# Kernel tuning notes

Measured on AMD Instinct MI355X. Metric: run time of the kernel, lower is better.

Reference implementation:

```python
import jax, jax.numpy as jnp
import numpy as np

D_MODEL = 1024
NHEAD = 16
HEAD_DIM = D_MODEL // NHEAD


def setup_inputs() -> dict:
    key = jax.random.key(0)
    kx, kw1, kb1, kw2, kb2 = jax.random.split(key, 5)
    x = jax.random.normal(kx, (4, 2048, D_MODEL), dtype=jnp.float32)
    s = 1.0 / np.sqrt(D_MODEL)
    W_qkv = jax.random.uniform(kw1, (D_MODEL, 3 * D_MODEL), jnp.float32, -s, s)
    b_qkv = jax.random.uniform(kb1, (3 * D_MODEL,), jnp.float32, -s, s)
    W_out = jax.random.uniform(kw2, (D_MODEL, D_MODEL), jnp.float32, -s, s)
    b_out = jax.random.uniform(kb2, (D_MODEL,), jnp.float32, -s, s)
    return {"x": x, "W_qkv": W_qkv, "b_qkv": b_qkv, "W_out": W_out, "b_out": b_out}


def reference(x, W_qkv, b_qkv, W_out, b_out):
    B, S, _ = x.shape
    scale = HEAD_DIM ** -0.5
    qkv = x @ W_qkv + b_qkv                               # [B,S,3*D]
    qkv = qkv.reshape(B, S, 3, NHEAD, HEAD_DIM)
    qkv = jnp.transpose(qkv, (2, 0, 3, 1, 4))             # [3,B,H,S,Dh]
    q, k, v = qkv[0], qkv[1], qkv[2]
    scores = jnp.einsum('bhsd,bhtd->bhst', q, k) * scale  # [B,H,S,S]
    attn = jax.nn.softmax(scores, axis=-1)
    out = jnp.einsum('bhst,bhtd->bhsd', attn, v)          # [B,H,S,Dh]
    out = jnp.transpose(out, (0, 2, 1, 3)).reshape(B, S, D_MODEL)
    return out @ W_out + b_out
```

## Files before the change

kernel.cpp:

```cpp
#include <hip/hip_runtime.h>
#include <hip/hip_bf16.h>

#define SEQ 2048
#define BATCH 4
#define DMODEL 1024
#define NHEAD 16

#define QK_SCALE_LOG2E 0.1803368801111137f

typedef __attribute__((ext_vector_type(8))) __bf16 bf16x8;
typedef __attribute__((ext_vector_type(4))) __bf16 bf16x4;
typedef __attribute__((ext_vector_type(4))) float f32x4;

__device__ __forceinline__ void gload_lds16(const void* g, void* l) {
    __builtin_amdgcn_global_load_lds(
        (const __attribute__((address_space(1))) void*)g,
        (__attribute__((address_space(3))) void*)l, 16, 0, 0);
}

__global__ __launch_bounds__(256) void cast_f32_to_bf16(
    const float* __restrict__ in, __bf16* __restrict__ out, int n4)
{
    int i = blockIdx.x * 256 + threadIdx.x;
    if (i >= n4) return;
    float4 v = reinterpret_cast<const float4*>(in)[i];
    bf16x4 o = { (__bf16)v.x, (__bf16)v.y, (__bf16)v.z, (__bf16)v.w };
    reinterpret_cast<bf16x4*>(out)[i] = o;
}

__global__ __launch_bounds__(256) void trans_w(
    const float* __restrict__ W, __bf16* __restrict__ WT, int K, int N)
{
    __shared__ float t[32][33];
    const int tid = threadIdx.x;
    const int n0 = blockIdx.x * 32, k0 = blockIdx.y * 32;
    const int tx = tid & 31, ty = tid >> 5;
    #pragma unroll
    for (int j = 0; j < 4; ++j)
        t[ty + 8*j][tx] = W[(size_t)(k0 + ty + 8*j) * N + n0 + tx];
    __syncthreads();
    #pragma unroll
    for (int j = 0; j < 4; ++j)
        WT[(size_t)(n0 + ty + 8*j) * K + k0 + tx] = (__bf16)t[tx][ty + 8*j];
}

__global__ __launch_bounds__(256) void gemm_qkv(
    const __bf16* __restrict__ A, const __bf16* __restrict__ BT,
    const float* __restrict__ bias,
    __bf16* __restrict__ Qb, __bf16* __restrict__ Kt, __bf16* __restrict__ Vt,
    int M, int N, int K)
{
    __shared__ __attribute__((aligned(128))) char As[2][8192];
    __shared__ __attribute__((aligned(128))) char Bs[2][8192];

    const int tid = threadIdx.x, wv = tid >> 6, ln = tid & 63;
    const int nwg = gridDim.x * gridDim.y;
    const int bid = blockIdx.y * gridDim.x + blockIdx.x;
    const int swz = (bid & 7) * (nwg >> 3) + (bid >> 3);
    const int rowBase = (swz / gridDim.x) * 128;
    const int colBase = (swz % gridDim.x) * 128;

    const int mq = (wv >> 1) * 64, nq = (wv & 1) * 64;
    const int lg = ln >> 4, lc = ln & 15;
    const int srow = ln >> 2;
    const int skoff = (ln & 3) * 8;

    const __bf16* asrc0 = A  + (size_t)(rowBase + (wv*2+0)*16 + srow) * K + skoff;
    const __bf16* asrc1 = A  + (size_t)(rowBase + (wv*2+1)*16 + srow) * K + skoff;
    const __bf16* bsrc0 = BT + (size_t)(colBase + (wv*2+0)*16 + srow) * K + skoff;
    const __bf16* bsrc1 = BT + (size_t)(colBase + (wv*2+1)*16 + srow) * K + skoff;

    #define GSTAGE(kt, buf) do {                                      \
        gload_lds16(asrc0 + (kt) * 32, As[buf] + (wv*2+0)*1024);      \
        gload_lds16(asrc1 + (kt) * 32, As[buf] + (wv*2+1)*1024);      \
        gload_lds16(bsrc0 + (kt) * 32, Bs[buf] + (wv*2+0)*1024);      \
        gload_lds16(bsrc1 + (kt) * 32, Bs[buf] + (wv*2+1)*1024);      \
    } while (0)

    const int nkt = K / 32;
    GSTAGE(0, 0);
    GSTAGE(1, 1);

    f32x4 acc[4][4] = {};

    for (int kt = 0; kt < nkt; ++kt) {
        const int cur = kt & 1;
        asm volatile("s_waitcnt vmcnt(4)" ::: "memory");
        __builtin_amdgcn_s_barrier();

        bf16x8 af[4], bf[4];
        #pragma unroll
        for (int m = 0; m < 4; ++m)
            af[m] = *(const bf16x8*)(As[cur] + (mq + m*16 + lc) * 64 + lg * 16);
        #pragma unroll
        for (int n = 0; n < 4; ++n)
            bf[n] = *(const bf16x8*)(Bs[cur] + (nq + n*16 + lc) * 64 + lg * 16);
        #pragma unroll
        for (int m = 0; m < 4; ++m)
            #pragma unroll
            for (int n = 0; n < 4; ++n)
                acc[m][n] = __builtin_amdgcn_mfma_f32_16x16x32_bf16(af[m], bf[n], acc[m][n], 0, 0, 0);

        __builtin_amdgcn_s_barrier();
        int cn = kt + 2;
        if (cn > nkt - 1) cn = nkt - 1;
        GSTAGE(cn, cur);
    }
    asm volatile("s_waitcnt vmcnt(0)" ::: "memory");
    #undef GSTAGE

    #pragma unroll
    for (int m = 0; m < 4; ++m) {
        int row0 = rowBase + mq + m * 16 + lg * 4;
        int b = row0 >> 11, s0 = row0 & 2047;
        #pragma unroll
        for (int n = 0; n < 4; ++n) {
            int col = colBase + nq + n * 16 + lc;
            float bv = bias[col];
            if (colBase < DMODEL) {
                #pragma unroll
                for (int r = 0; r < 4; ++r)
                    Qb[(size_t)(row0 + r) * DMODEL + col] =
                        (__bf16)((acc[m][n][r] + bv) * QK_SCALE_LOG2E);
            } else if (colBase < 2 * DMODEL) {
                int h = (col >> 6) & 15, d = col & 63;
                __bf16* kp = &Kt[((size_t)(b * 16 + h) * SEQ + s0) * 64 + d];
                #pragma unroll
                for (int r = 0; r < 4; ++r)
                    kp[r * 64] = (__bf16)(acc[m][n][r] + bv);
            } else {
                int h = (col >> 6) & 15, d = col & 63;
                int sp = (s0 & ~63) | (s0 & 32) | ((s0 & 12) << 1) | ((s0 & 16) >> 2);
                bf16x4 vv = { (__bf16)(acc[m][n][0] + bv), (__bf16)(acc[m][n][1] + bv),
                              (__bf16)(acc[m][n][2] + bv), (__bf16)(acc[m][n][3] + bv) };
                *(bf16x4*)&Vt[((size_t)(b * 16 + h) * 64 + d) * SEQ + sp] = vv;
            }
        }
    }
}

__global__ __launch_bounds__(256) void gemm_out(
    const __bf16* __restrict__ A, const __bf16* __restrict__ BT,
    const float* __restrict__ bias, float* __restrict__ Cout,
    int M, int N, int K)
{
    __shared__ __attribute__((aligned(128))) char As[2][8192];
    __shared__ __attribute__((aligned(128))) char Bs[2][8192];

    const int tid = threadIdx.x, wv = tid >> 6, ln = tid & 63;
    const int nwg = gridDim.x * gridDim.y;
    const int bid = blockIdx.y * gridDim.x + blockIdx.x;
    const int swz = (bid & 7) * (nwg >> 3) + (bid >> 3);
    const int rowBase = (swz / gridDim.x) * 128;
    const int colBase = (swz % gridDim.x) * 128;

    const int mq = (wv >> 1) * 64, nq = (wv & 1) * 64;
    const int lg = ln >> 4, lc = ln & 15;
    const int srow = ln >> 2;
    const int skoff = (ln & 3) * 8;

    const __bf16* asrc0 = A  + (size_t)(rowBase + (wv*2+0)*16 + srow) * K + skoff;
    const __bf16* asrc1 = A  + (size_t)(rowBase + (wv*2+1)*16 + srow) * K + skoff;
    const __bf16* bsrc0 = BT + (size_t)(colBase + (wv*2+0)*16 + srow) * K + skoff;
    const __bf16* bsrc1 = BT + (size_t)(colBase + (wv*2+1)*16 + srow) * K + skoff;

    #define GSTAGE(kt, buf) do {                                      \
        gload_lds16(asrc0 + (kt) * 32, As[buf] + (wv*2+0)*1024);      \
        gload_lds16(asrc1 + (kt) * 32, As[buf] + (wv*2+1)*1024);      \
        gload_lds16(bsrc0 + (kt) * 32, Bs[buf] + (wv*2+0)*1024);      \
        gload_lds16(bsrc1 + (kt) * 32, Bs[buf] + (wv*2+1)*1024);      \
    } while (0)

    const int nkt = K / 32;
    GSTAGE(0, 0);
    GSTAGE(1, 1);

    f32x4 acc[4][4] = {};

    for (int kt = 0; kt < nkt; ++kt) {
        const int cur = kt & 1;
        asm volatile("s_waitcnt vmcnt(4)" ::: "memory");
        __builtin_amdgcn_s_barrier();

        bf16x8 af[4], bf[4];
        #pragma unroll
        for (int m = 0; m < 4; ++m)
            af[m] = *(const bf16x8*)(As[cur] + (mq + m*16 + lc) * 64 + lg * 16);
        #pragma unroll
        for (int n = 0; n < 4; ++n)
            bf[n] = *(const bf16x8*)(Bs[cur] + (nq + n*16 + lc) * 64 + lg * 16);
        #pragma unroll
        for (int m = 0; m < 4; ++m)
            #pragma unroll
            for (int n = 0; n < 4; ++n)
                acc[m][n] = __builtin_amdgcn_mfma_f32_16x16x32_bf16(af[m], bf[n], acc[m][n], 0, 0, 0);

        __builtin_amdgcn_s_barrier();
        int cn = kt + 2;
        if (cn > nkt - 1) cn = nkt - 1;
        GSTAGE(cn, cur);
    }
    asm volatile("s_waitcnt vmcnt(0)" ::: "memory");
    #undef GSTAGE

    #pragma unroll
    for (int m = 0; m < 4; ++m) {
        int row0 = rowBase + mq + m * 16 + lg * 4;
        #pragma unroll
        for (int n = 0; n < 4; ++n) {
            int col = colBase + nq + n * 16 + lc;
            float bv = bias[col];
            #pragma unroll
            for (int r = 0; r < 4; ++r)
                Cout[(size_t)(row0 + r) * N + col] = acc[m][n][r] + bv;
        }
    }
}

__global__ __launch_bounds__(256, 4) void attn_mfma(
    const __bf16* __restrict__ Qb,
    const __bf16* __restrict__ Kt,
    const __bf16* __restrict__ Vt,
    __bf16* __restrict__ attn_out)
{
    __shared__ __attribute__((aligned(128))) char Ks[2][8192];
    __shared__ __attribute__((aligned(128))) char Vs[2][8192];

    const int tid = threadIdx.x, wv = tid >> 6, ln = tid & 63;
    const int swzb = (blockIdx.x & 7) * 128 + (blockIdx.x >> 3);
    const int qt = swzb & 15;
    const int bh = swzb >> 4;
    const int b = bh >> 4, h = bh & 15;
    const int lg = ln >> 4, lc = ln & 15;

    bf16x8 qf[2][2];
    #pragma unroll
    for (int m = 0; m < 2; ++m) {
        int qrow = qt * 128 + wv * 32 + m * 16 + lc;
        #pragma unroll
        for (int t = 0; t < 2; ++t)
            qf[m][t] = *(const bf16x8*)&Qb[((size_t)b * SEQ + qrow) * DMODEL + h * 64 + t * 32 + lg * 8];
    }

    f32x4 Oacc[4][2] = {};
    float lrun[2] = {0.f, 0.f};

    const int strow = ln >> 3;
    const int sl8 = ln & 7;
    const int r0 = (wv * 2 + 0) * 8 + strow;
    const int r1 = (wv * 2 + 1) * 8 + strow;
    const int s0 = sl8 ^ (r0 & 7);
    const int s1 = sl8 ^ (r1 & 7);
    const __bf16* ksrc0 = &Kt[((size_t)bh * SEQ + r0) * 64 + s0 * 8];
    const __bf16* ksrc1 = &Kt[((size_t)bh * SEQ + r1) * 64 + s1 * 8];
    const __bf16* vsrc0 = &Vt[((size_t)bh * 64 + r0) * SEQ + s0 * 8];
    const __bf16* vsrc1 = &Vt[((size_t)bh * 64 + r1) * SEQ + s1 * 8];

    #define STAGE(c, buf) do {                                                   \
        gload_lds16(ksrc0 + (size_t)(c) * 4096, Ks[buf] + (wv*2+0)*1024);        \
        gload_lds16(ksrc1 + (size_t)(c) * 4096, Ks[buf] + (wv*2+1)*1024);        \
        gload_lds16(vsrc0 + (size_t)(c) * 64,   Vs[buf] + (wv*2+0)*1024);        \
        gload_lds16(vsrc1 + (size_t)(c) * 64,   Vs[buf] + (wv*2+1)*1024);        \
    } while (0)

    STAGE(0, 0);
    STAGE(1, 1);

    for (int c = 0; c < SEQ / 64; ++c) {
        const int cur = c & 1;
        asm volatile("s_waitcnt vmcnt(4)" ::: "memory");
        __builtin_amdgcn_s_barrier();

        const char* Kc = Ks[cur];
        const char* Vc = Vs[cur];

        f32x4 Sacc[4][2] = {};
        #pragma unroll
        for (int n = 0; n < 4; ++n) {
            int row = n * 16 + lc;
            int xo = (row & 7) << 4;
            #pragma unroll
            for (int t = 0; t < 2; ++t) {
                bf16x8 kf = *(const bf16x8*)(Kc + row * 128 + ((t * 64 + lg * 16) ^ xo));
                #pragma unroll
                for (int m = 0; m < 2; ++m)
                    Sacc[n][m] = __builtin_amdgcn_mfma_f32_16x16x32_bf16(kf, qf[m][t], Sacc[n][m], 0, 0, 0);
            }
        }

        bf16x8 w[2][2];
        #pragma unroll
        for (int m = 0; m < 2; ++m) {
            float psum = 0.f;
            #pragma unroll
            for (int n = 0; n < 4; ++n) {
                #pragma unroll
                for (int r = 0; r < 4; ++r) {
                    float v = __builtin_amdgcn_exp2f(Sacc[n][m][r]);
                    psum += v;
                    w[m][n >> 1][(n & 1) * 4 + r] = (__bf16)v;
                }
            }
            lrun[m] += psum;
        }

        #pragma unroll
        for (int t = 0; t < 2; ++t) {
            #pragma unroll
            for (int n = 0; n < 4; ++n) {
                int row = n * 16 + lc;
                bf16x8 vf = *(const bf16x8*)(Vc + row * 128 + ((t * 64 + lg * 16) ^ ((row & 7) << 4)));
                #pragma unroll
                for (int m = 0; m < 2; ++m)
                    Oacc[n][m] = __builtin_amdgcn_mfma_f32_16x16x32_bf16(vf, w[m][t], Oacc[n][m], 0, 0, 0);
            }
        }

        __builtin_amdgcn_s_barrier();
        int cn = c + 2;
        if (cn > SEQ / 64 - 1) cn = SEQ / 64 - 1;
        STAGE(cn, cur);
    }
    asm volatile("s_waitcnt vmcnt(0)" ::: "memory");
    #undef STAGE

    #pragma unroll
    for (int m = 0; m < 2; ++m) {
        float l = lrun[m];
        l += __shfl_xor(l, 16);
        l += __shfl_xor(l, 32);
        float inv = 1.0f / l;
        int qrow = qt * 128 + wv * 32 + m * 16 + lc;
        #pragma unroll
        for (int n = 0; n < 4; ++n) {
            bf16x4 o = { (__bf16)(Oacc[n][m][0] * inv), (__bf16)(Oacc[n][m][1] * inv),
                         (__bf16)(Oacc[n][m][2] * inv), (__bf16)(Oacc[n][m][3] * inv) };
            *(bf16x4*)&attn_out[((size_t)b * SEQ + qrow) * DMODEL + h * 64 + n * 16 + lg * 4] = o;
        }
    }
}

extern "C" void kernel_launch(void* const* d_in, const int* in_sizes, int n_in,
                              void* d_out, int out_size, void* d_ws, size_t ws_size,
                              hipStream_t stream) {
    (void)in_sizes; (void)n_in; (void)out_size; (void)ws_size;
    const float* x     = (const float*)d_in[0];
    const float* W_qkv = (const float*)d_in[1];
    const float* b_qkv = (const float*)d_in[2];
    const float* W_out = (const float*)d_in[3];
    const float* b_out = (const float*)d_in[4];
    float* out = (float*)d_out;

    char* ws = (char*)d_ws;
    __bf16* xb    = (__bf16*)(ws);
    __bf16* WqkvT = (__bf16*)(ws + ((size_t)16 << 20));
    __bf16* WoutT = (__bf16*)(ws + ((size_t)22 << 20));
    __bf16* Qb    = (__bf16*)(ws + ((size_t)24 << 20));
    __bf16* Kt    = (__bf16*)(ws + ((size_t)40 << 20));
    __bf16* Vt    = (__bf16*)(ws + ((size_t)56 << 20));
    __bf16* attnb = (__bf16*)(ws + ((size_t)72 << 20));

    const int M = BATCH * SEQ;

    cast_f32_to_bf16<<<dim3(M * DMODEL / 4 / 256), 256, 0, stream>>>(x, xb, M * DMODEL / 4);
    trans_w<<<dim3(3 * DMODEL / 32, DMODEL / 32), 256, 0, stream>>>(W_qkv, WqkvT, DMODEL, 3 * DMODEL);
    trans_w<<<dim3(DMODEL / 32, DMODEL / 32), 256, 0, stream>>>(W_out, WoutT, DMODEL, DMODEL);

    gemm_qkv<<<dim3(3 * DMODEL / 128, M / 128), 256, 0, stream>>>(
        xb, WqkvT, b_qkv, Qb, Kt, Vt, M, 3 * DMODEL, DMODEL);

    attn_mfma<<<dim3(BATCH * NHEAD * (SEQ / 128)), 256, 0, stream>>>(Qb, Kt, Vt, attnb);

    gemm_out<<<dim3(DMODEL / 128, M / 128), 256, 0, stream>>>(
        attnb, WoutT, b_out, out, M, DMODEL, DMODEL);
}
```

Measured before the change: 189.4 us.

## Merge prep kernels into one launch and compute softmax row sums with MFMA

Folds the input cast kernel and the two weight-transpose kernels into a single prep_inputs launch, dispatching on block index, so two kernel launches and their gaps go away. Separately, the attention kernel now accumulates the softmax denominator with an extra MFMA against a vector of ones, replacing per-lane scalar adds and cross-lane shuffles. This adds matrix work per tile and sums the bf16-rounded weights rather than the fp32 values, which may change accuracy slightly.

```diff
diff --git a/kernel.cpp b/kernel.cpp
--- a/kernel.cpp
+++ b/kernel.cpp
@@ -18,22 +18,32 @@
         (__attribute__((address_space(3))) void*)l, 16, 0, 0);
 }
 
-__global__ __launch_bounds__(256) void cast_f32_to_bf16(
-    const float* __restrict__ in, __bf16* __restrict__ out, int n4)
-{
-    int i = blockIdx.x * 256 + threadIdx.x;
-    if (i >= n4) return;
-    float4 v = reinterpret_cast<const float4*>(in)[i];
-    bf16x4 o = { (__bf16)v.x, (__bf16)v.y, (__bf16)v.z, (__bf16)v.w };
-    reinterpret_cast<bf16x4*>(out)[i] = o;
-}
-
-__global__ __launch_bounds__(256) void trans_w(
-    const float* __restrict__ W, __bf16* __restrict__ WT, int K, int N)
+__global__ __launch_bounds__(256) void prep_inputs(
+    const float* __restrict__ x, __bf16* __restrict__ xb,
+    const float* __restrict__ W_qkv, __bf16* __restrict__ WqkvT,
+    const float* __restrict__ W_out, __bf16* __restrict__ WoutT)
 {
     __shared__ float t[32][33];
     const int tid = threadIdx.x;
-    const int n0 = blockIdx.x * 32, k0 = blockIdx.y * 32;
+    const int bid = blockIdx.x;
+
+    if (bid < 8192) {
+        int i = bid * 256 + tid;
+        float4 v = reinterpret_cast<const float4*>(x)[i];
+        bf16x4 o = { (__bf16)v.x, (__bf16)v.y, (__bf16)v.z, (__bf16)v.w };
+        reinterpret_cast<bf16x4*>(xb)[i] = o;
+        return;
+    }
+    const float* W; __bf16* WT; int N, bx, by;
+    if (bid < 8192 + 3072) {
+        int idx = bid - 8192;
+        W = W_qkv; WT = WqkvT; N = 3072; bx = idx % 96; by = idx / 96;
+    } else {
+        int idx = bid - 11264;
+        W = W_out; WT = WoutT; N = 1024; bx = idx & 31; by = idx >> 5;
+    }
+    const int K = 1024;
+    const int n0 = bx * 32, k0 = by * 32;
     const int tx = tid & 31, ty = tid >> 5;
     #pragma unroll
     for (int j = 0; j < 4; ++j)
@@ -242,8 +252,11 @@
             qf[m][t] = *(const bf16x8*)&Qb[((size_t)b * SEQ + qrow) * DMODEL + h * 64 + t * 32 + lg * 8];
     }
 
+    const __bf16 one = (__bf16)1.0f;
+    const bf16x8 ones8 = { one, one, one, one, one, one, one, one };
+
     f32x4 Oacc[4][2] = {};
-    float lrun[2] = {0.f, 0.f};
+    f32x4 lacc[2] = {};
 
     const int strow = ln >> 3;
     const int sl8 = ln & 7;
@@ -290,19 +303,19 @@
 
         bf16x8 w[2][2];
         #pragma unroll
-        for (int m = 0; m < 2; ++m) {
-            float psum = 0.f;
-            #pragma unroll
-            for (int n = 0; n < 4; ++n) {
-                #pragma unroll
-                for (int r = 0; r < 4; ++r) {
-                    float v = __builtin_amdgcn_exp2f(Sacc[n][m][r]);
-                    psum += v;
-                    w[m][n >> 1][(n & 1) * 4 + r] = (__bf16)v;
-                }
-            }
-            lrun[m] += psum;
-        }
+        for (int m = 0; m < 2; ++m)
+            #pragma unroll
+            for (int n = 0; n < 4; ++n)
+                #pragma unroll
+                for (int r = 0; r < 4; ++r)
+                    w[m][n >> 1][(n & 1) * 4 + r] =
+                        (__bf16)__builtin_amdgcn_exp2f(Sacc[n][m][r]);
+
+        #pragma unroll
+        for (int m = 0; m < 2; ++m)
+            #pragma unroll
+            for (int t = 0; t < 2; ++t)
+                lacc[m] = __builtin_amdgcn_mfma_f32_16x16x32_bf16(ones8, w[m][t], lacc[m], 0, 0, 0);
 
         #pragma unroll
         for (int t = 0; t < 2; ++t) {
@@ -326,10 +339,7 @@
 
     #pragma unroll
     for (int m = 0; m < 2; ++m) {
-        float l = lrun[m];
-        l += __shfl_xor(l, 16);
-        l += __shfl_xor(l, 32);
-        float inv = 1.0f / l;
+        float inv = 1.0f / lacc[m][0];
         int qrow = qt * 128 + wv * 32 + m * 16 + lc;
         #pragma unroll
         for (int n = 0; n < 4; ++n) {
@@ -362,9 +372,7 @@
 
     const int M = BATCH * SEQ;
 
-    cast_f32_to_bf16<<<dim3(M * DMODEL / 4 / 256), 256, 0, stream>>>(x, xb, M * DMODEL / 4);
-    trans_w<<<dim3(3 * DMODEL / 32, DMODEL / 32), 256, 0, stream>>>(W_qkv, WqkvT, DMODEL, 3 * DMODEL);
-    trans_w<<<dim3(DMODEL / 32, DMODEL / 32), 256, 0, stream>>>(W_out, WoutT, DMODEL, DMODEL);
+    prep_inputs<<<dim3(12288), 256, 0, stream>>>(x, xb, W_qkv, WqkvT, W_out, WoutT);
 
     gemm_qkv<<<dim3(3 * DMODEL / 128, M / 128), 256, 0, stream>>>(
         xb, WqkvT, b_qkv, Qb, Kt, Vt, M, 3 * DMODEL, DMODEL);
```

After: 178.9 us. -5.6%, faster.
